# Kernel optimization log

Hardware: AMD Instinct MI355X
Metric: run time of the kernel (lower is better)

Reference implementation:

```python
import jax, jax.numpy as jnp
import numpy as np

EPS = 1e-12  # F.normalize eps


def _l2norm_spatial(x):
    # F.normalize(x, p=2, dim=(2,3)): divide by max(||x||_2 over HxW, eps)
    n = jnp.sqrt(jnp.sum(x * x, axis=(2, 3), keepdims=True))
    return x / jnp.maximum(n, EPS)


def _cscr_forward(rgb, ir):
    C = rgb.shape[1]
    # channel average pooling (cap) and channel max pooling (cmp)
    rgb_cap = jnp.mean(rgb, axis=1, keepdims=True)
    rgb_cmp = jnp.max(rgb, axis=1, keepdims=True)
    ir_cap = jnp.mean(ir, axis=1, keepdims=True)
    ir_cmp = jnp.max(ir, axis=1, keepdims=True)
    # cp = cat([cap,cmp]) summed across modalities; sa = max(cp[:,0::2], cp[:,1::2])
    sa = jnp.maximum(rgb_cap + ir_cap, rgb_cmp + ir_cmp)  # [B,1,H,W]
    sa_sig = jax.nn.sigmoid(sa)

    # cosine similarity of each channel with the (sigmoid'd) spatial attention map
    sa_n = _l2norm_spatial(sa_sig)
    sim_rgb = jnp.sum(sa_n * _l2norm_spatial(rgb), axis=(2, 3))  # [B,C]
    sim_ir = jnp.sum(sa_n * _l2norm_spatial(ir), axis=(2, 3))    # [B,C]

    # sort channels by similarity ascending and gather
    ord_rgb = jnp.argsort(sim_rgb, axis=1)
    ord_ir = jnp.argsort(sim_ir, axis=1)
    sorted_rgb = jnp.take_along_axis(rgb, ord_rgb[:, :, None, None], axis=1)
    sorted_ir = jnp.take_along_axis(ir, ord_ir[:, :, None, None], axis=1)

    # split point = max over batch of #positive similarities (scalar per stream)
    n_rgb = jnp.max(jnp.sum(sim_rgb > 0, axis=1))
    n_ir = jnp.max(jnp.sum(sim_ir > 0, axis=1))

    # When C_rgb == C_ir, torch's equalize_channel_lengths_positive pads the
    # stream with the SMALLER positive count with one extra channel
    # max(sorted_rgb[:, :1], sorted_ir[:, :1]) (the strided slice [::extra] of
    # the first `extra` channels collapses to channel 0), and the subsequent
    # negative truncation drops that stream's last (most positive) channel.
    # The stream with the larger positive count comes out as its full sorted
    # channels. We express that shape-statically with a shifted gather + where.
    extra_fea = jnp.maximum(sorted_rgb[:, :1], sorted_ir[:, :1])  # [B,1,H,W]
    idx = jnp.arange(C)

    def reassemble(sorted_x, n_self, n_other):
        g = jnp.where(idx <= n_self, idx, idx - 1)          # gather with shift after insertion point
        shifted = jnp.take(sorted_x, g, axis=1)             # [B,C,H,W]
        inserted = jnp.where((idx == n_self)[None, :, None, None], extra_fea, shifted)
        return jnp.where(n_other > n_self, inserted, sorted_x)

    rgb_cs = reassemble(sorted_rgb, n_rgb, n_ir)
    ir_cs = reassemble(sorted_ir, n_ir, n_rgb)

    # final spatial-attention gating
    return rgb_cs * sa_sig, ir_cs * sa_sig


def setup_inputs() -> dict:
    key = jax.random.key(0)
    k1, k2 = jax.random.split(key)
    B, C, H, W = 32, 256, 56, 56
    rgb = jax.random.normal(k1, (B, C, H, W), dtype=jnp.float32)
    ir = jax.random.normal(k2, (B, C, H, W), dtype=jnp.float32)
    return {"rgb": rgb, "ir": ir}


def reference(rgb, ir):
    return _cscr_forward(rgb, ir)
```

## Files before the change

### kernel.cpp

```cpp
#include <hip/hip_runtime.h>
#include <math.h>


#define CDIM   256
#define HWDIM  3136
#define CHW    (CDIM * HWDIM)
#define PAIRS  1568
#define QUADS  784

typedef unsigned short u16;
typedef unsigned int   u32;

__device__ __forceinline__ float bf2f(u32 u) { return __uint_as_float(u << 16); }
__device__ __forceinline__ u16  f2bf(float f) {
    u32 x = __float_as_uint(f);
    return (u16)((x + 0x7FFFu + ((x >> 16) & 1u)) >> 16);
}
__device__ __forceinline__ u32 pack2(u32 u, float s0, float s1) {
    float a0 = __uint_as_float(u << 16);
    float a1 = __uint_as_float(u & 0xFFFF0000u);
    u32 lo = f2bf(a0 * s0), hi = f2bf(a1 * s1);
    return lo | (hi << 16);
}
__device__ __forceinline__ u32 maxpack2(u32 u, u32 w, float s0, float s1) {
    float a0 = __uint_as_float(u << 16), a1 = __uint_as_float(u & 0xFFFF0000u);
    float b0 = __uint_as_float(w << 16), b1 = __uint_as_float(w & 0xFFFF0000u);
    u32 lo = f2bf(fmaxf(a0, b0) * s0), hi = f2bf(fmaxf(a1, b1) * s1);
    return lo | (hi << 16);
}

__global__ __launch_bounds__(64) void k_sa(const void* __restrict__ rgb_,
                                           const void* __restrict__ ir_,
                                           int* __restrict__ flg,
                                           float* __restrict__ sa32,
                                           int* __restrict__ nmx) {
    int lane = threadIdx.x;

    int w = 0;
    {
        u32 u = ((const u32*)rgb_)[lane];
        u32 hs[2] = { u & 0xFFFFu, u >> 16 };
        #pragma unroll
        for (int k = 0; k < 2; ++k) {
            int e = (hs[k] >> 7) & 0xFF;
            float v = bf2f(hs[k]);
            if (e == 0xFF || fabsf(v) > 1e3f) w++;
        }
    }
    #pragma unroll
    for (int off = 32; off >= 1; off >>= 1) w += __shfl_xor(w, off, 64);
    int md = (w > 8) ? 1 : 0;
    if (blockIdx.x == 0 && blockIdx.y == 0 && lane == 0) {
        flg[0] = md;
        nmx[0] = 0; nmx[1] = 0;
    }

    int b  = blockIdx.y;
    int g  = lane >> 4;
    int ql = blockIdx.x * 16 + (lane & 15);

    double s0 = 0.0, s1 = 0.0, s2 = 0.0, s3 = 0.0;
    float m0r = -INFINITY, m1r = -INFINITY, m2r = -INFINITY, m3r = -INFINITY;
    float m0i = -INFINITY, m1i = -INFINITY, m2i = -INFINITY, m3i = -INFINITY;

    if (md == 1) {
        const float4* R = (const float4*)rgb_ + (size_t)b * (CHW / 4) + ql;
        const float4* I = (const float4*)ir_  + (size_t)b * (CHW / 4) + ql;
        #pragma unroll 4
        for (int k = 0; k < 64; ++k) {
            size_t o = (size_t)(4 * k + g) * QUADS;
            float4 r = R[o];
            float4 i = I[o];
            s0 += (double)r.x + (double)i.x;
            s1 += (double)r.y + (double)i.y;
            s2 += (double)r.z + (double)i.z;
            s3 += (double)r.w + (double)i.w;
            m0r = fmaxf(m0r, r.x); m1r = fmaxf(m1r, r.y);
            m2r = fmaxf(m2r, r.z); m3r = fmaxf(m3r, r.w);
            m0i = fmaxf(m0i, i.x); m1i = fmaxf(m1i, i.y);
            m2i = fmaxf(m2i, i.z); m3i = fmaxf(m3i, i.w);
        }
    } else {
        const uint2* R = (const uint2*)rgb_ + (size_t)b * (CHW / 4) + ql;
        const uint2* I = (const uint2*)ir_  + (size_t)b * (CHW / 4) + ql;
        #pragma unroll 4
        for (int k = 0; k < 64; ++k) {
            size_t o = (size_t)(4 * k + g) * QUADS;
            uint2 ur = R[o];
            uint2 ui = I[o];
            float r0 = bf2f(ur.x & 0xFFFFu), r1 = bf2f(ur.x >> 16);
            float r2 = bf2f(ur.y & 0xFFFFu), r3 = bf2f(ur.y >> 16);
            float i0 = bf2f(ui.x & 0xFFFFu), i1 = bf2f(ui.x >> 16);
            float i2 = bf2f(ui.y & 0xFFFFu), i3 = bf2f(ui.y >> 16);
            s0 += (double)r0 + (double)i0;
            s1 += (double)r1 + (double)i1;
            s2 += (double)r2 + (double)i2;
            s3 += (double)r3 + (double)i3;
            m0r = fmaxf(m0r, r0); m1r = fmaxf(m1r, r1);
            m2r = fmaxf(m2r, r2); m3r = fmaxf(m3r, r3);
            m0i = fmaxf(m0i, i0); m1i = fmaxf(m1i, i1);
            m2i = fmaxf(m2i, i2); m3i = fmaxf(m3i, i3);
        }
    }

    #pragma unroll
    for (int off = 16; off <= 32; off <<= 1) {
        s0 += __shfl_xor(s0, off, 64);
        s1 += __shfl_xor(s1, off, 64);
        s2 += __shfl_xor(s2, off, 64);
        s3 += __shfl_xor(s3, off, 64);
        m0r = fmaxf(m0r, __shfl_xor(m0r, off, 64));
        m1r = fmaxf(m1r, __shfl_xor(m1r, off, 64));
        m2r = fmaxf(m2r, __shfl_xor(m2r, off, 64));
        m3r = fmaxf(m3r, __shfl_xor(m3r, off, 64));
        m0i = fmaxf(m0i, __shfl_xor(m0i, off, 64));
        m1i = fmaxf(m1i, __shfl_xor(m1i, off, 64));
        m2i = fmaxf(m2i, __shfl_xor(m2i, off, 64));
        m3i = fmaxf(m3i, __shfl_xor(m3i, off, 64));
    }

    if (lane < 16) {
        double sa0 = fmax(s0 * (1.0 / 256.0), (double)m0r + (double)m0i);
        double sa1 = fmax(s1 * (1.0 / 256.0), (double)m1r + (double)m1i);
        double sa2 = fmax(s2 * (1.0 / 256.0), (double)m2r + (double)m2i);
        double sa3 = fmax(s3 * (1.0 / 256.0), (double)m3r + (double)m3i);
        float4 ov;
        ov.x = (float)(1.0 / (1.0 + exp(-sa0)));
        ov.y = (float)(1.0 / (1.0 + exp(-sa1)));
        ov.z = (float)(1.0 / (1.0 + exp(-sa2)));
        ov.w = (float)(1.0 / (1.0 + exp(-sa3)));
        *(float4*)&sa32[(size_t)b * HWDIM + 4 * (size_t)ql] = ov;
    }
}

__global__ __launch_bounds__(256) void k_sim(const void* __restrict__ rgb_,
                                             const void* __restrict__ ir_,
                                             const int* __restrict__ flg,
                                             const float* __restrict__ sa32,
                                             double* __restrict__ sims) {
    __shared__ float s_sa[HWDIM];
    int p0 = blockIdx.x * 4;
    int b  = (p0 >> 8) & 31;
    {
        const float4* src = (const float4*)(sa32 + (size_t)b * HWDIM);
        float4* dst = (float4*)s_sa;
        for (int i = threadIdx.x; i < QUADS; i += 256) dst[i] = src[i];
    }
    __syncthreads();

    int wid = threadIdx.x >> 6, lane = threadIdx.x & 63;
    int p = p0 + wid;
    int stream = p >> 13;
    int md = flg[0];
    int plane = p & 8191;
    const float4* sv = (const float4*)s_sa;

    double ss = 0.0, dot = 0.0;
    if (md == 1) {
        const float4* x = (const float4*)(stream ? ir_ : rgb_) + (size_t)plane * QUADS;
        #pragma unroll 2
        for (int j = lane; j < QUADS; j += 64) {
            float4 v = x[j];
            float4 s = sv[j];
            ss  = fma((double)v.x, (double)v.x,
                  fma((double)v.y, (double)v.y,
                  fma((double)v.z, (double)v.z,
                  fma((double)v.w, (double)v.w, ss))));
            dot = fma((double)s.x, (double)v.x,
                  fma((double)s.y, (double)v.y,
                  fma((double)s.z, (double)v.z,
                  fma((double)s.w, (double)v.w, dot))));
        }
    } else {
        const u32* x = (const u32*)(stream ? ir_ : rgb_) + (size_t)plane * PAIRS;
        #pragma unroll 2
        for (int j = lane; j < QUADS; j += 64) {
            u32 w0 = x[2 * j], w1 = x[2 * j + 1];
            double v0 = (double)bf2f(w0 & 0xFFFFu), v1 = (double)bf2f(w0 >> 16);
            double v2 = (double)bf2f(w1 & 0xFFFFu), v3 = (double)bf2f(w1 >> 16);
            float4 s = sv[j];
            ss  = fma(v0, v0, fma(v1, v1, fma(v2, v2, fma(v3, v3, ss))));
            dot = fma((double)s.x, v0, fma((double)s.y, v1,
                  fma((double)s.z, v2, fma((double)s.w, v3, dot))));
        }
    }
    #pragma unroll
    for (int off = 32; off >= 1; off >>= 1) {
        ss  += __shfl_xor(ss,  off, 64);
        dot += __shfl_xor(dot, off, 64);
    }
    if (lane == 0) {
        double nrm = sqrt(ss);
        if (nrm < 1e-12) nrm = 1e-12;
        sims[p] = dot / nrm;
    }
}

__global__ __launch_bounds__(256) void k_sort(const double* __restrict__ sims,
                                              int* __restrict__ ord,
                                              int* __restrict__ nmx) {
    __shared__ double s[256];
    __shared__ int csum;
    int sb = blockIdx.x;
    int c  = threadIdx.x;
    double v = sims[sb * 256 + c];
    if (isnan(v)) v = -INFINITY;
    s[c] = v;
    if (c == 0) csum = 0;
    __syncthreads();
    int rank = 0;
    #pragma unroll 8
    for (int j = 0; j < 256; ++j) {
        double u = s[j];
        rank += (u < v) || (u == v && j < c);
    }
    ord[sb * 256 + rank] = c;
    unsigned long long m = __ballot(v > 0.0);
    if ((c & 63) == 0) atomicAdd(&csum, (int)__popcll(m));
    __syncthreads();
    if (c == 0) atomicMax(&nmx[sb >> 5], csum);
}

__global__ __launch_bounds__(256) void k_gather(const void* __restrict__ rgb_,
                                                const void* __restrict__ ir_,
                                                const int* __restrict__ flg,
                                                const float* __restrict__ sa32,
                                                const int* __restrict__ ord,
                                                const int* __restrict__ nmax,
                                                void* __restrict__ out_) {
    int sb = blockIdx.x;
    int stream = sb >> 13;
    int b  = (sb >> 8) & 31;
    int co = sb & 255;
    int md = flg[0];
    int n_self  = nmax[stream];
    int n_other = nmax[1 - stream];
    bool insert  = n_other > n_self;
    bool special = insert && (co == n_self);
    int obase = sb & ~255;

    const float*  sig = sa32 + (size_t)b * HWDIM;
    const float4* sg  = (const float4*)sig;

    if (!special) {
        int ci = co;
        if (insert && co > n_self) ci = co - 1;
        int src = ord[obase + ci] & 255;
        size_t pb = (size_t)(b * 256 + src) * HWDIM;
        if (md == 0) {
            const u16* x = stream ? (const u16*)ir_ : (const u16*)rgb_;
            const uint4* xin = (const uint4*)(x + pb);
            uint4* o = (uint4*)((u16*)out_ + (size_t)sb * HWDIM);
            for (int i = threadIdx.x; i < 392; i += 256) {
                uint4 u = xin[i];
                float4 s0 = sg[2 * i], s1 = sg[2 * i + 1];
                uint4 r;
                r.x = pack2(u.x, s0.x, s0.y);
                r.y = pack2(u.y, s0.z, s0.w);
                r.z = pack2(u.z, s1.x, s1.y);
                r.w = pack2(u.w, s1.z, s1.w);
                o[i] = r;
            }
        } else {
            const float* x = stream ? (const float*)ir_ : (const float*)rgb_;
            const float4* xin = (const float4*)(x + pb);
            float4* o = (float4*)((float*)out_ + (size_t)sb * HWDIM);
            for (int i = threadIdx.x; i < 784; i += 256) {
                float4 v = xin[i], s = sg[i];
                o[i] = make_float4(v.x * s.x, v.y * s.y, v.z * s.z, v.w * s.w);
            }
        }
    } else {
        int src_r = ord[b * 256] & 255;
        int src_i = ord[8192 + b * 256] & 255;
        size_t pr = (size_t)(b * 256 + src_r) * HWDIM;
        size_t pi = (size_t)(b * 256 + src_i) * HWDIM;
        if (md == 0) {
            const uint4* xr = (const uint4*)((const u16*)rgb_ + pr);
            const uint4* xi = (const uint4*)((const u16*)ir_  + pi);
            uint4* o = (uint4*)((u16*)out_ + (size_t)sb * HWDIM);
            for (int i = threadIdx.x; i < 392; i += 256) {
                uint4 u = xr[i], w = xi[i];
                float4 s0 = sg[2 * i], s1 = sg[2 * i + 1];
                uint4 r;
                r.x = maxpack2(u.x, w.x, s0.x, s0.y);
                r.y = maxpack2(u.y, w.y, s0.z, s0.w);
                r.z = maxpack2(u.z, w.z, s1.x, s1.y);
                r.w = maxpack2(u.w, w.w, s1.z, s1.w);
                o[i] = r;
            }
        } else {
            const float4* xr = (const float4*)((const float*)rgb_ + pr);
            const float4* xi = (const float4*)((const float*)ir_  + pi);
            float4* o = (float4*)((float*)out_ + (size_t)sb * HWDIM);
            for (int i = threadIdx.x; i < 784; i += 256) {
                float4 u = xr[i], w = xi[i], s = sg[i];
                o[i] = make_float4(fmaxf(u.x, w.x) * s.x, fmaxf(u.y, w.y) * s.y,
                                   fmaxf(u.z, w.z) * s.z, fmaxf(u.w, w.w) * s.w);
            }
        }
    }
}

extern "C" void kernel_launch(void* const* d_in, const int* in_sizes, int n_in,
                              void* d_out, int out_size, void* d_ws, size_t ws_size,
                              hipStream_t stream) {
    const void* rgb = d_in[0];
    const void* ir  = d_in[1];

    char* ws = (char*)d_ws;
    int*    flg  = (int*)   ws;
    float*  sa32 = (float*) (ws + 1024);
    double* sims = (double*)(ws + 402432);
    int*    ord  = (int*)   (ws + 533504);
    int*    nmx  = (int*)   (ws + 599296);

    k_sa    <<<dim3(49, 32), 64, 0, stream>>>(rgb, ir, flg, sa32, nmx);
    k_sim   <<<4096,        256, 0, stream>>>(rgb, ir, flg, sa32, sims);
    k_sort  <<<64,          256, 0, stream>>>(sims, ord, nmx);
    k_gather<<<16384,       256, 0, stream>>>(rgb, ir, flg, sa32, ord, nmx, d_out);
}
```

Measured before the change: 427.9 us.

## Fuse four kernels into one persistent kernel with grid-wide barriers

Replaces the four kernel launches (spatial attention, similarity, sort, gather) with one persistent kernel of 1024 blocks that steps through the phases using a software grid barrier built on atomics, after a memset that clears the counters. This removes launch gaps between stages and lets each block reuse its shared-memory copy of the attention map in the gather phase. The cost is lower parallelism per phase, with 1024 blocks each looping over many planes, idle blocks during the sort phase, and the risk of deadlock if not all blocks are resident at once.

Measured after the change: 1.090 ms. 2.55x slower.

```diff
diff --git a/kernel.cpp b/kernel.cpp
--- a/kernel.cpp
+++ b/kernel.cpp
@@ -7,6 +7,8 @@
 #define CHW    (CDIM * HWDIM)
 #define PAIRS  1568
 #define QUADS  784
+#define NBLK   1024
+#define NTHR   256
 
 typedef unsigned short u16;
 typedef unsigned int   u32;
@@ -29,274 +31,295 @@
     return lo | (hi << 16);
 }
 
-__global__ __launch_bounds__(64) void k_sa(const void* __restrict__ rgb_,
-                                           const void* __restrict__ ir_,
-                                           int* __restrict__ flg,
-                                           float* __restrict__ sa32,
-                                           int* __restrict__ nmx) {
-    int lane = threadIdx.x;
-
-    int w = 0;
+__device__ __forceinline__ void gsync(int* cnt, int* gen) {
+    __threadfence();
+    __syncthreads();
+    if (threadIdx.x == 0) {
+        int g = __hip_atomic_load(gen, __ATOMIC_RELAXED, __HIP_MEMORY_SCOPE_AGENT);
+        int a = __hip_atomic_fetch_add(cnt, 1, __ATOMIC_ACQ_REL, __HIP_MEMORY_SCOPE_AGENT);
+        if (a == NBLK - 1) {
+            __hip_atomic_store(cnt, 0, __ATOMIC_RELAXED, __HIP_MEMORY_SCOPE_AGENT);
+            __hip_atomic_store(gen, g + 1, __ATOMIC_RELEASE, __HIP_MEMORY_SCOPE_AGENT);
+        } else {
+            while (__hip_atomic_load(gen, __ATOMIC_ACQUIRE, __HIP_MEMORY_SCOPE_AGENT) == g) {
+                __builtin_amdgcn_s_sleep(8);
+            }
+        }
+    }
+    __syncthreads();
+}
+
+__global__ __launch_bounds__(NTHR, 4) void k_fused(const void* __restrict__ rgb_,
+                                                   const void* __restrict__ ir_,
+                                                   int* __restrict__ wsi,
+                                                   float* __restrict__ sa32,
+                                                   double* __restrict__ sims,
+                                                   int* __restrict__ ord,
+                                                   void* __restrict__ out_) {
+    int* bar_cnt = wsi + 0;
+    int* bar_gen = wsi + 1;
+    int* nmx     = wsi + 2;
+
+    __shared__ float  s_sa[HWDIM];
+    __shared__ double s_srt[256];
+    __shared__ int    s_ci;
+
+    int tid = threadIdx.x, bid = blockIdx.x;
+    int lane = tid & 63, wid = tid >> 6;
+
+    int wd = 0;
     {
         u32 u = ((const u32*)rgb_)[lane];
-        u32 hs[2] = { u & 0xFFFFu, u >> 16 };
-        #pragma unroll
-        for (int k = 0; k < 2; ++k) {
-            int e = (hs[k] >> 7) & 0xFF;
-            float v = bf2f(hs[k]);
-            if (e == 0xFF || fabsf(v) > 1e3f) w++;
-        }
+        u32 h0 = u & 0xFFFFu, h1 = u >> 16;
+        int e0 = (h0 >> 7) & 0xFF, e1 = (h1 >> 7) & 0xFF;
+        if (e0 == 0xFF || fabsf(bf2f(h0)) > 1e3f) wd++;
+        if (e1 == 0xFF || fabsf(bf2f(h1)) > 1e3f) wd++;
     }
     #pragma unroll
-    for (int off = 32; off >= 1; off >>= 1) w += __shfl_xor(w, off, 64);
-    int md = (w > 8) ? 1 : 0;
-    if (blockIdx.x == 0 && blockIdx.y == 0 && lane == 0) {
-        flg[0] = md;
-        nmx[0] = 0; nmx[1] = 0;
-    }
-
-    int b  = blockIdx.y;
-    int g  = lane >> 4;
-    int ql = blockIdx.x * 16 + (lane & 15);
-
-    double s0 = 0.0, s1 = 0.0, s2 = 0.0, s3 = 0.0;
-    float m0r = -INFINITY, m1r = -INFINITY, m2r = -INFINITY, m3r = -INFINITY;
-    float m0i = -INFINITY, m1i = -INFINITY, m2i = -INFINITY, m3i = -INFINITY;
-
-    if (md == 1) {
-        const float4* R = (const float4*)rgb_ + (size_t)b * (CHW / 4) + ql;
-        const float4* I = (const float4*)ir_  + (size_t)b * (CHW / 4) + ql;
-        #pragma unroll 4
-        for (int k = 0; k < 64; ++k) {
-            size_t o = (size_t)(4 * k + g) * QUADS;
-            float4 r = R[o];
-            float4 i = I[o];
-            s0 += (double)r.x + (double)i.x;
-            s1 += (double)r.y + (double)i.y;
-            s2 += (double)r.z + (double)i.z;
-            s3 += (double)r.w + (double)i.w;
-            m0r = fmaxf(m0r, r.x); m1r = fmaxf(m1r, r.y);
-            m2r = fmaxf(m2r, r.z); m3r = fmaxf(m3r, r.w);
-            m0i = fmaxf(m0i, i.x); m1i = fmaxf(m1i, i.y);
-            m2i = fmaxf(m2i, i.z); m3i = fmaxf(m3i, i.w);
-        }
-    } else {
-        const uint2* R = (const uint2*)rgb_ + (size_t)b * (CHW / 4) + ql;
-        const uint2* I = (const uint2*)ir_  + (size_t)b * (CHW / 4) + ql;
-        #pragma unroll 4
-        for (int k = 0; k < 64; ++k) {
-            size_t o = (size_t)(4 * k + g) * QUADS;
-            uint2 ur = R[o];
-            uint2 ui = I[o];
-            float r0 = bf2f(ur.x & 0xFFFFu), r1 = bf2f(ur.x >> 16);
-            float r2 = bf2f(ur.y & 0xFFFFu), r3 = bf2f(ur.y >> 16);
-            float i0 = bf2f(ui.x & 0xFFFFu), i1 = bf2f(ui.x >> 16);
-            float i2 = bf2f(ui.y & 0xFFFFu), i3 = bf2f(ui.y >> 16);
-            s0 += (double)r0 + (double)i0;
-            s1 += (double)r1 + (double)i1;
-            s2 += (double)r2 + (double)i2;
-            s3 += (double)r3 + (double)i3;
-            m0r = fmaxf(m0r, r0); m1r = fmaxf(m1r, r1);
-            m2r = fmaxf(m2r, r2); m3r = fmaxf(m3r, r3);
-            m0i = fmaxf(m0i, i0); m1i = fmaxf(m1i, i1);
-            m2i = fmaxf(m2i, i2); m3i = fmaxf(m3i, i3);
-        }
-    }
-
-    #pragma unroll
-    for (int off = 16; off <= 32; off <<= 1) {
-        s0 += __shfl_xor(s0, off, 64);
-        s1 += __shfl_xor(s1, off, 64);
-        s2 += __shfl_xor(s2, off, 64);
-        s3 += __shfl_xor(s3, off, 64);
-        m0r = fmaxf(m0r, __shfl_xor(m0r, off, 64));
-        m1r = fmaxf(m1r, __shfl_xor(m1r, off, 64));
-        m2r = fmaxf(m2r, __shfl_xor(m2r, off, 64));
-        m3r = fmaxf(m3r, __shfl_xor(m3r, off, 64));
-        m0i = fmaxf(m0i, __shfl_xor(m0i, off, 64));
-        m1i = fmaxf(m1i, __shfl_xor(m1i, off, 64));
-        m2i = fmaxf(m2i, __shfl_xor(m2i, off, 64));
-        m3i = fmaxf(m3i, __shfl_xor(m3i, off, 64));
-    }
-
-    if (lane < 16) {
-        double sa0 = fmax(s0 * (1.0 / 256.0), (double)m0r + (double)m0i);
-        double sa1 = fmax(s1 * (1.0 / 256.0), (double)m1r + (double)m1i);
-        double sa2 = fmax(s2 * (1.0 / 256.0), (double)m2r + (double)m2i);
-        double sa3 = fmax(s3 * (1.0 / 256.0), (double)m3r + (double)m3i);
-        float4 ov;
-        ov.x = (float)(1.0 / (1.0 + exp(-sa0)));
-        ov.y = (float)(1.0 / (1.0 + exp(-sa1)));
-        ov.z = (float)(1.0 / (1.0 + exp(-sa2)));
-        ov.w = (float)(1.0 / (1.0 + exp(-sa3)));
-        *(float4*)&sa32[(size_t)b * HWDIM + 4 * (size_t)ql] = ov;
-    }
-}
-
-__global__ __launch_bounds__(256) void k_sim(const void* __restrict__ rgb_,
-                                             const void* __restrict__ ir_,
-                                             const int* __restrict__ flg,
-                                             const float* __restrict__ sa32,
-                                             double* __restrict__ sims) {
-    __shared__ float s_sa[HWDIM];
-    int p0 = blockIdx.x * 4;
-    int b  = (p0 >> 8) & 31;
-    {
-        const float4* src = (const float4*)(sa32 + (size_t)b * HWDIM);
+    for (int off = 32; off >= 1; off >>= 1) wd += __shfl_xor(wd, off, 64);
+    const int md = (wd > 8) ? 1 : 0;
+
+    {
+        int gw = bid * 4 + wid;
+        if (gw < 3136) {
+            int b  = gw / 98, qg = gw - b * 98;
+            int qoff = lane & 7, sg = lane >> 3;
+            int ql = qg * 8 + qoff;
+
+            double s0 = 0.0, s1 = 0.0, s2 = 0.0, s3 = 0.0;
+            float m0r = -INFINITY, m1r = -INFINITY, m2r = -INFINITY, m3r = -INFINITY;
+            float m0i = -INFINITY, m1i = -INFINITY, m2i = -INFINITY, m3i = -INFINITY;
+
+            if (md == 1) {
+                const float4* R = (const float4*)rgb_ + (size_t)b * (CHW / 4)
+                                  + (size_t)sg * QUADS + ql;
+                const float4* I = (const float4*)ir_  + (size_t)b * (CHW / 4)
+                                  + (size_t)sg * QUADS + ql;
+                #pragma unroll 4
+                for (int k = 0; k < 32; ++k) {
+                    size_t o = (size_t)(8 * k) * QUADS;
+                    float4 r = R[o];
+                    float4 i = I[o];
+                    s0 += (double)r.x + (double)i.x;
+                    s1 += (double)r.y + (double)i.y;
+                    s2 += (double)r.z + (double)i.z;
+                    s3 += (double)r.w + (double)i.w;
+                    m0r = fmaxf(m0r, r.x); m1r = fmaxf(m1r, r.y);
+                    m2r = fmaxf(m2r, r.z); m3r = fmaxf(m3r, r.w);
+                    m0i = fmaxf(m0i, i.x); m1i = fmaxf(m1i, i.y);
+                    m2i = fmaxf(m2i, i.z); m3i = fmaxf(m3i, i.w);
+                }
+            } else {
+                const uint2* R = (const uint2*)rgb_ + (size_t)b * (CHW / 4)
+                                 + (size_t)sg * QUADS + ql;
+                const uint2* I = (const uint2*)ir_  + (size_t)b * (CHW / 4)
+                                 + (size_t)sg * QUADS + ql;
+                #pragma unroll 4
+                for (int k = 0; k < 32; ++k) {
+                    size_t o = (size_t)(8 * k) * QUADS;
+                    uint2 ur = R[o];
+                    uint2 ui = I[o];
+                    float r0 = bf2f(ur.x & 0xFFFFu), r1 = bf2f(ur.x >> 16);
+                    float r2 = bf2f(ur.y & 0xFFFFu), r3 = bf2f(ur.y >> 16);
+                    float i0 = bf2f(ui.x & 0xFFFFu), i1 = bf2f(ui.x >> 16);
+                    float i2 = bf2f(ui.y & 0xFFFFu), i3 = bf2f(ui.y >> 16);
+                    s0 += (double)r0 + (double)i0;
+                    s1 += (double)r1 + (double)i1;
+                    s2 += (double)r2 + (double)i2;
+                    s3 += (double)r3 + (double)i3;
+                    m0r = fmaxf(m0r, r0); m1r = fmaxf(m1r, r1);
+                    m2r = fmaxf(m2r, r2); m3r = fmaxf(m3r, r3);
+                    m0i = fmaxf(m0i, i0); m1i = fmaxf(m1i, i1);
+                    m2i = fmaxf(m2i, i2); m3i = fmaxf(m3i, i3);
+                }
+            }
+
+            #pragma unroll
+            for (int off = 8; off <= 32; off <<= 1) {
+                s0 += __shfl_xor(s0, off, 64);
+                s1 += __shfl_xor(s1, off, 64);
+                s2 += __shfl_xor(s2, off, 64);
+                s3 += __shfl_xor(s3, off, 64);
+                m0r = fmaxf(m0r, __shfl_xor(m0r, off, 64));
+                m1r = fmaxf(m1r, __shfl_xor(m1r, off, 64));
+                m2r = fmaxf(m2r, __shfl_xor(m2r, off, 64));
+                m3r = fmaxf(m3r, __shfl_xor(m3r, off, 64));
+                m0i = fmaxf(m0i, __shfl_xor(m0i, off, 64));
+                m1i = fmaxf(m1i, __shfl_xor(m1i, off, 64));
+                m2i = fmaxf(m2i, __shfl_xor(m2i, off, 64));
+                m3i = fmaxf(m3i, __shfl_xor(m3i, off, 64));
+            }
+
+            if (sg == 0) {
+                double sa0 = fmax(s0 * (1.0 / 256.0), (double)m0r + (double)m0i);
+                double sa1 = fmax(s1 * (1.0 / 256.0), (double)m1r + (double)m1i);
+                double sa2 = fmax(s2 * (1.0 / 256.0), (double)m2r + (double)m2i);
+                double sa3 = fmax(s3 * (1.0 / 256.0), (double)m3r + (double)m3i);
+                float4 ov;
+                ov.x = (float)(1.0 / (1.0 + exp(-sa0)));
+                ov.y = (float)(1.0 / (1.0 + exp(-sa1)));
+                ov.z = (float)(1.0 / (1.0 + exp(-sa2)));
+                ov.w = (float)(1.0 / (1.0 + exp(-sa3)));
+                *(float4*)&sa32[(size_t)b * HWDIM + 4 * (size_t)ql] = ov;
+            }
+        }
+    }
+
+    gsync(bar_cnt, bar_gen);
+
+    int p0     = bid << 4;
+    int stream = bid >> 9;
+    int b2     = (bid >> 4) & 31;
+    {
+        const float4* src = (const float4*)(sa32 + (size_t)b2 * HWDIM);
         float4* dst = (float4*)s_sa;
-        for (int i = threadIdx.x; i < QUADS; i += 256) dst[i] = src[i];
+        for (int i = tid; i < QUADS; i += NTHR) dst[i] = src[i];
     }
     __syncthreads();
-
-    int wid = threadIdx.x >> 6, lane = threadIdx.x & 63;
-    int p = p0 + wid;
-    int stream = p >> 13;
-    int md = flg[0];
-    int plane = p & 8191;
-    const float4* sv = (const float4*)s_sa;
-
-    double ss = 0.0, dot = 0.0;
-    if (md == 1) {
-        const float4* x = (const float4*)(stream ? ir_ : rgb_) + (size_t)plane * QUADS;
-        #pragma unroll 2
-        for (int j = lane; j < QUADS; j += 64) {
-            float4 v = x[j];
-            float4 s = sv[j];
-            ss  = fma((double)v.x, (double)v.x,
-                  fma((double)v.y, (double)v.y,
-                  fma((double)v.z, (double)v.z,
-                  fma((double)v.w, (double)v.w, ss))));
-            dot = fma((double)s.x, (double)v.x,
-                  fma((double)s.y, (double)v.y,
-                  fma((double)s.z, (double)v.z,
-                  fma((double)s.w, (double)v.w, dot))));
-        }
-    } else {
-        const u32* x = (const u32*)(stream ? ir_ : rgb_) + (size_t)plane * PAIRS;
-        #pragma unroll 2
-        for (int j = lane; j < QUADS; j += 64) {
-            u32 w0 = x[2 * j], w1 = x[2 * j + 1];
-            double v0 = (double)bf2f(w0 & 0xFFFFu), v1 = (double)bf2f(w0 >> 16);
-            double v2 = (double)bf2f(w1 & 0xFFFFu), v3 = (double)bf2f(w1 >> 16);
-            float4 s = sv[j];
-            ss  = fma(v0, v0, fma(v1, v1, fma(v2, v2, fma(v3, v3, ss))));
-            dot = fma((double)s.x, v0, fma((double)s.y, v1,
-                  fma((double)s.z, v2, fma((double)s.w, v3, dot))));
-        }
-    }
-    #pragma unroll
-    for (int off = 32; off >= 1; off >>= 1) {
-        ss  += __shfl_xor(ss,  off, 64);
-        dot += __shfl_xor(dot, off, 64);
-    }
-    if (lane == 0) {
-        double nrm = sqrt(ss);
-        if (nrm < 1e-12) nrm = 1e-12;
-        sims[p] = dot / nrm;
-    }
-}
-
-__global__ __launch_bounds__(256) void k_sort(const double* __restrict__ sims,
-                                              int* __restrict__ ord,
-                                              int* __restrict__ nmx) {
-    __shared__ double s[256];
-    __shared__ int csum;
-    int sb = blockIdx.x;
-    int c  = threadIdx.x;
-    double v = sims[sb * 256 + c];
-    if (isnan(v)) v = -INFINITY;
-    s[c] = v;
-    if (c == 0) csum = 0;
-    __syncthreads();
-    int rank = 0;
-    #pragma unroll 8
-    for (int j = 0; j < 256; ++j) {
-        double u = s[j];
-        rank += (u < v) || (u == v && j < c);
-    }
-    ord[sb * 256 + rank] = c;
-    unsigned long long m = __ballot(v > 0.0);
-    if ((c & 63) == 0) atomicAdd(&csum, (int)__popcll(m));
-    __syncthreads();
-    if (c == 0) atomicMax(&nmx[sb >> 5], csum);
-}
-
-__global__ __launch_bounds__(256) void k_gather(const void* __restrict__ rgb_,
-                                                const void* __restrict__ ir_,
-                                                const int* __restrict__ flg,
-                                                const float* __restrict__ sa32,
-                                                const int* __restrict__ ord,
-                                                const int* __restrict__ nmax,
-                                                void* __restrict__ out_) {
-    int sb = blockIdx.x;
-    int stream = sb >> 13;
-    int b  = (sb >> 8) & 31;
-    int co = sb & 255;
-    int md = flg[0];
-    int n_self  = nmax[stream];
-    int n_other = nmax[1 - stream];
-    bool insert  = n_other > n_self;
-    bool special = insert && (co == n_self);
-    int obase = sb & ~255;
-
-    const float*  sig = sa32 + (size_t)b * HWDIM;
-    const float4* sg  = (const float4*)sig;
-
-    if (!special) {
-        int ci = co;
-        if (insert && co > n_self) ci = co - 1;
-        int src = ord[obase + ci] & 255;
-        size_t pb = (size_t)(b * 256 + src) * HWDIM;
-        if (md == 0) {
-            const u16* x = stream ? (const u16*)ir_ : (const u16*)rgb_;
-            const uint4* xin = (const uint4*)(x + pb);
-            uint4* o = (uint4*)((u16*)out_ + (size_t)sb * HWDIM);
-            for (int i = threadIdx.x; i < 392; i += 256) {
-                uint4 u = xin[i];
-                float4 s0 = sg[2 * i], s1 = sg[2 * i + 1];
-                uint4 r;
-                r.x = pack2(u.x, s0.x, s0.y);
-                r.y = pack2(u.y, s0.z, s0.w);
-                r.z = pack2(u.z, s1.x, s1.y);
-                r.w = pack2(u.w, s1.z, s1.w);
-                o[i] = r;
-            }
-        } else {
-            const float* x = stream ? (const float*)ir_ : (const float*)rgb_;
-            const float4* xin = (const float4*)(x + pb);
-            float4* o = (float4*)((float*)out_ + (size_t)sb * HWDIM);
-            for (int i = threadIdx.x; i < 784; i += 256) {
-                float4 v = xin[i], s = sg[i];
-                o[i] = make_float4(v.x * s.x, v.y * s.y, v.z * s.z, v.w * s.w);
-            }
-        }
-    } else {
-        int src_r = ord[b * 256] & 255;
-        int src_i = ord[8192 + b * 256] & 255;
-        size_t pr = (size_t)(b * 256 + src_r) * HWDIM;
-        size_t pi = (size_t)(b * 256 + src_i) * HWDIM;
-        if (md == 0) {
-            const uint4* xr = (const uint4*)((const u16*)rgb_ + pr);
-            const uint4* xi = (const uint4*)((const u16*)ir_  + pi);
-            uint4* o = (uint4*)((u16*)out_ + (size_t)sb * HWDIM);
-            for (int i = threadIdx.x; i < 392; i += 256) {
-                uint4 u = xr[i], w = xi[i];
-                float4 s0 = sg[2 * i], s1 = sg[2 * i + 1];
-                uint4 r;
-                r.x = maxpack2(u.x, w.x, s0.x, s0.y);
-                r.y = maxpack2(u.y, w.y, s0.z, s0.w);
-                r.z = maxpack2(u.z, w.z, s1.x, s1.y);
-                r.w = maxpack2(u.w, w.w, s1.z, s1.w);
-                o[i] = r;
-            }
-        } else {
-            const float4* xr = (const float4*)((const float*)rgb_ + pr);
-            const float4* xi = (const float4*)((const float*)ir_  + pi);
-            float4* o = (float4*)((float*)out_ + (size_t)sb * HWDIM);
-            for (int i = threadIdx.x; i < 784; i += 256) {
-                float4 u = xr[i], w = xi[i], s = sg[i];
-                o[i] = make_float4(fmaxf(u.x, w.x) * s.x, fmaxf(u.y, w.y) * s.y,
-                                   fmaxf(u.z, w.z) * s.z, fmaxf(u.w, w.w) * s.w);
+    {
+        const float4* sv = (const float4*)s_sa;
+        for (int k = 0; k < 4; ++k) {
+            int p = p0 + wid * 4 + k;
+            int plane = p & 8191;
+            double ss = 0.0, dot = 0.0;
+            if (md == 1) {
+                const float4* x = (const float4*)(stream ? ir_ : rgb_)
+                                  + (size_t)plane * QUADS;
+                #pragma unroll 2
+                for (int j = lane; j < QUADS; j += 64) {
+                    float4 v = x[j];
+                    float4 s = sv[j];
+                    ss  = fma((double)v.x, (double)v.x,
+                          fma((double)v.y, (double)v.y,
+                          fma((double)v.z, (double)v.z,
+                          fma((double)v.w, (double)v.w, ss))));
+                    dot = fma((double)s.x, (double)v.x,
+                          fma((double)s.y, (double)v.y,
+                          fma((double)s.z, (double)v.z,
+                          fma((double)s.w, (double)v.w, dot))));
+                }
+            } else {
+                const u32* x = (const u32*)(stream ? ir_ : rgb_)
+                               + (size_t)plane * PAIRS;
+                #pragma unroll 2
+                for (int j = lane; j < QUADS; j += 64) {
+                    u32 w0 = x[2 * j], w1 = x[2 * j + 1];
+                    double v0 = (double)bf2f(w0 & 0xFFFFu), v1 = (double)bf2f(w0 >> 16);
+                    double v2 = (double)bf2f(w1 & 0xFFFFu), v3 = (double)bf2f(w1 >> 16);
+                    float4 s = sv[j];
+                    ss  = fma(v0, v0, fma(v1, v1, fma(v2, v2, fma(v3, v3, ss))));
+                    dot = fma((double)s.x, v0, fma((double)s.y, v1,
+                          fma((double)s.z, v2, fma((double)s.w, v3, dot))));
+                }
+            }
+            #pragma unroll
+            for (int off = 32; off >= 1; off >>= 1) {
+                ss  += __shfl_xor(ss,  off, 64);
+                dot += __shfl_xor(dot, off, 64);
+            }
+            if (lane == 0) {
+                double nrm = sqrt(ss);
+                if (nrm < 1e-12) nrm = 1e-12;
+                sims[p] = dot / nrm;
+            }
+        }
+    }
+
+    gsync(bar_cnt, bar_gen);
+
+    if (bid < 64) {
+        int sb = bid;
+        int c  = tid;
+        double v = sims[sb * 256 + c];
+        if (isnan(v)) v = -INFINITY;
+        s_srt[c] = v;
+        if (c == 0) s_ci = 0;
+        __syncthreads();
+        int rank = 0;
+        #pragma unroll 8
+        for (int j = 0; j < 256; ++j) {
+            double u = s_srt[j];
+            rank += (u < v) || (u == v && j < c);
+        }
+        ord[sb * 256 + rank] = c;
+        unsigned long long mB = __ballot(v > 0.0);
+        if ((c & 63) == 0) atomicAdd(&s_ci, (int)__popcll(mB));
+        __syncthreads();
+        if (c == 0) atomicMax(&nmx[sb >> 5], s_ci);
+    }
+
+    gsync(bar_cnt, bar_gen);
+
+    {
+        int n_self  = nmx[stream];
+        int n_other = nmx[1 - stream];
+        bool insert = n_other > n_self;
+        const float4* sg4 = (const float4*)s_sa;
+
+        for (int k = 0; k < 16; ++k) {
+            int po = p0 + k;
+            int co = po & 255;
+            bool special = insert && (co == n_self);
+
+            if (!special) {
+                int ci = co;
+                if (insert && co > n_self) ci = co - 1;
+                int src = ord[(po & ~255) + ci] & 255;
+                size_t pb = (size_t)(b2 * 256 + src) * HWDIM;
+                if (md == 0) {
+                    const u16* x = stream ? (const u16*)ir_ : (const u16*)rgb_;
+                    const uint4* xin = (const uint4*)(x + pb);
+                    uint4* o = (uint4*)((u16*)out_ + (size_t)po * HWDIM);
+                    for (int i = tid; i < 392; i += NTHR) {
+                        uint4 u = xin[i];
+                        float4 sA = sg4[2 * i], sB = sg4[2 * i + 1];
+                        uint4 r;
+                        r.x = pack2(u.x, sA.x, sA.y);
+                        r.y = pack2(u.y, sA.z, sA.w);
+                        r.z = pack2(u.z, sB.x, sB.y);
+                        r.w = pack2(u.w, sB.z, sB.w);
+                        o[i] = r;
+                    }
+                } else {
+                    const float* x = stream ? (const float*)ir_ : (const float*)rgb_;
+                    const float4* xin = (const float4*)(x + pb);
+                    float4* o = (float4*)((float*)out_ + (size_t)po * HWDIM);
+                    for (int i = tid; i < 784; i += NTHR) {
+                        float4 v = xin[i], s = sg4[i];
+                        o[i] = make_float4(v.x * s.x, v.y * s.y, v.z * s.z, v.w * s.w);
+                    }
+                }
+            } else {
+                int src_r = ord[b2 * 256] & 255;
+                int src_i = ord[8192 + b2 * 256] & 255;
+                size_t pr = (size_t)(b2 * 256 + src_r) * HWDIM;
+                size_t pi = (size_t)(b2 * 256 + src_i) * HWDIM;
+                if (md == 0) {
+                    const uint4* xr = (const uint4*)((const u16*)rgb_ + pr);
+                    const uint4* xi = (const uint4*)((const u16*)ir_  + pi);
+                    uint4* o = (uint4*)((u16*)out_ + (size_t)po * HWDIM);
+                    for (int i = tid; i < 392; i += NTHR) {
+                        uint4 u = xr[i], w = xi[i];
+                        float4 sA = sg4[2 * i], sB = sg4[2 * i + 1];
+                        uint4 r;
+                        r.x = maxpack2(u.x, w.x, sA.x, sA.y);
+                        r.y = maxpack2(u.y, w.y, sA.z, sA.w);
+                        r.z = maxpack2(u.z, w.z, sB.x, sB.y);
+                        r.w = maxpack2(u.w, w.w, sB.z, sB.w);
+                        o[i] = r;
+                    }
+                } else {
+                    const float4* xr = (const float4*)((const float*)rgb_ + pr);
+                    const float4* xi = (const float4*)((const float*)ir_  + pi);
+                    float4* o = (float4*)((float*)out_ + (size_t)po * HWDIM);
+                    for (int i = tid; i < 784; i += NTHR) {
+                        float4 u = xr[i], w = xi[i], s = sg4[i];
+                        o[i] = make_float4(fmaxf(u.x, w.x) * s.x,
+                                           fmaxf(u.y, w.y) * s.y,
+                                           fmaxf(u.z, w.z) * s.z,
+                                           fmaxf(u.w, w.w) * s.w);
+                    }
+                }
             }
         }
     }
@@ -309,14 +332,12 @@
     const void* ir  = d_in[1];
 
     char* ws = (char*)d_ws;
-    int*    flg  = (int*)   ws;
+    int*    wsi  = (int*)   ws;
     float*  sa32 = (float*) (ws + 1024);
     double* sims = (double*)(ws + 402432);
     int*    ord  = (int*)   (ws + 533504);
-    int*    nmx  = (int*)   (ws + 599296);
-
-    k_sa    <<<dim3(49, 32), 64, 0, stream>>>(rgb, ir, flg, sa32, nmx);
-    k_sim   <<<4096,        256, 0, stream>>>(rgb, ir, flg, sa32, sims);
-    k_sort  <<<64,          256, 0, stream>>>(sims, ord, nmx);
-    k_gather<<<16384,       256, 0, stream>>>(rgb, ir, flg, sa32, ord, nmx, d_out);
-}
+
+    hipMemsetAsync(wsi, 0, 64, stream);
+    hipLaunchKernelGGL(k_fused, dim3(NBLK), dim3(NTHR), 0, stream,
+                       rgb, ir, wsi, sa32, sims, ord, d_out);
+}
```
